# Optimization experiments

Measured on AMD Instinct MI355X. Metric: run time of the kernel, lower is better.

Reference implementation:

```python
import jax, jax.numpy as jnp
import numpy as np

N, K, D = 8192, 512, 4096

def setup_inputs() -> dict:
    key = jax.random.key(0)
    k1, k2, k3 = jax.random.split(key, 3)
    features = jax.random.normal(k1, (N, K), dtype=jnp.float32)
    w = jax.random.normal(k2, (D, N), dtype=jnp.float32)
    E = jax.random.normal(k3, (K, D), dtype=jnp.float32) / np.sqrt(K)  # embed_matrix (k x d)
    b = jnp.zeros((D,), dtype=jnp.float32)  # bias initialized to zeros in the module
    return {"features": features, "w": w, "E": E, "b": b}

def reference(features, w, E, b):
    # Linear: y = features @ E + b  -> (N, D)   (torch weight is E.mT, so x @ W.T == x @ E)
    y = features @ E + b
    # diag(y @ w): equivalent to row-wise dot products, same math without the NxN matmul
    return jnp.einsum("nd,dn->n", y, w)
```

## Files before the change

### kernel.cpp

```cpp
#include <hip/hip_runtime.h>

#define N_DIM 8192
#define K_DIM 512
#define D_DIM 4096

typedef __bf16 bf16x8 __attribute__((ext_vector_type(8)));
typedef float  f32x16 __attribute__((ext_vector_type(16)));
typedef unsigned short u16x8 __attribute__((ext_vector_type(8)));

__device__ __forceinline__ unsigned short f2bf(float f) {
    union { float f; unsigned int u; } v; v.f = f;
    unsigned int r = v.u + 0x7FFF + ((v.u >> 16) & 1);
    return (unsigned short)(r >> 16);
}

__global__ __launch_bounds__(256) void transpose_E(const float* __restrict__ E,
                                                   unsigned short* __restrict__ ETf) {
    __shared__ float tile[64][65];
    const int d0 = blockIdx.x * 64;
    const int k0 = blockIdx.y * 64;
    const int tid = threadIdx.x;
    {
        const int r  = tid / 16;
        const int c4 = (tid % 16) * 4;
#pragma unroll
        for (int p = 0; p < 4; ++p) {
            int k = p * 16 + r;
            float4 v = *reinterpret_cast<const float4*>(E + (size_t)(k0 + k) * D_DIM + d0 + c4);
            tile[k][c4 + 0] = v.x; tile[k][c4 + 1] = v.y;
            tile[k][c4 + 2] = v.z; tile[k][c4 + 3] = v.w;
        }
    }
    __syncthreads();
    const int lane = tid & 63;
    const int w    = tid >> 6;
    const int dl5  = lane & 31;
    const int k8h  = lane >> 5;
#pragma unroll
    for (int q = 0; q < 2; ++q) {
        u16x8 o;
#pragma unroll
        for (int j = 0; j < 8; ++j)
            o[j] = f2bf(tile[w * 16 + k8h * 8 + j][q * 32 + dl5]);
        const int frag = ((d0 >> 5) + q) * 32 + (k0 >> 4) + w;
        *reinterpret_cast<u16x8*>(ETf + (size_t)frag * 512 + lane * 8) = o;
    }
}

__global__ __launch_bounds__(256) void convert_F(const float* __restrict__ F,
                                                 unsigned short* __restrict__ FB) {
    const int idx8 = (blockIdx.x * 256 + threadIdx.x) * 8;
    float4 a = *reinterpret_cast<const float4*>(F + idx8);
    float4 b = *reinterpret_cast<const float4*>(F + idx8 + 4);
    u16x8 o;
    o[0] = f2bf(a.x); o[1] = f2bf(a.y); o[2] = f2bf(a.z); o[3] = f2bf(a.w);
    o[4] = f2bf(b.x); o[5] = f2bf(b.y); o[6] = f2bf(b.z); o[7] = f2bf(b.w);
    *reinterpret_cast<u16x8*>(FB + idx8) = o;
}

__global__ __launch_bounds__(256) void gemm_fused(const unsigned short* __restrict__ FB,
                                                  const float* __restrict__ W,
                                                  const unsigned short* __restrict__ ETf,
                                                  const float* __restrict__ B,
                                                  float* __restrict__ out) {
    __shared__ unsigned short Bsh[2 * 128 * 32];

    const int tid  = threadIdx.x;
    const int wave = tid >> 6;
    const int lane = tid & 63;
    const int wy   = wave >> 1;
    const int wx   = wave & 1;
    const int l31  = lane & 31;
    const int half = lane >> 5;

    const int f   = blockIdx.x + ((int)gridDim.x) * blockIdx.y;
    const int xcd = f & 7;
    const int s   = f >> 3;
    const int ntile = (xcd & 3) * 16 + (s & 15);
    const int dtile = (xcd >> 2) * 16 + (s >> 4);
    const int n0 = ntile * 128;
    const int d0 = dtile * 128;

    f32x16 acc[2][2] = {};

    const unsigned short* pa0 = ETf + (size_t)((d0 >> 5) + wy * 2 + 0) * 16384 + lane * 8;
    const unsigned short* pa1 = ETf + (size_t)((d0 >> 5) + wy * 2 + 1) * 16384 + lane * 8;

    const int srow   = lane >> 2;
    const int schunk = (((lane & 3) ^ ((srow >> 1) & 3)) * 8);

    for (int kt = 0; kt < K_DIM / 64; ++kt) {
        const int kb = kt * 64;
#pragma unroll
        for (int p = 0; p < 2; ++p) {
#pragma unroll
            for (int jj = 0; jj < 2; ++jj) {
                const int j = wave * 2 + jj;
                const unsigned short* gb =
                    FB + (size_t)(n0 + j * 16 + srow) * K_DIM + kb + p * 32 + schunk;
                __builtin_amdgcn_global_load_lds(
                    (const __attribute__((address_space(1))) void*)gb,
                    (__attribute__((address_space(3))) void*)(Bsh + p * 4096 + j * 512),
                    16, 0, 0);
            }
        }
        __syncthreads();

#pragma unroll
        for (int ks = 0; ks < 4; ++ks) {
            const int p = ks >> 1;
            const int c = (ks & 1) * 2 + half;
            bf16x8 af[2], bf[2];
            af[0] = *reinterpret_cast<const bf16x8*>(pa0 + (kt * 4 + ks) * 512);
            af[1] = *reinterpret_cast<const bf16x8*>(pa1 + (kt * 4 + ks) * 512);
#pragma unroll
            for (int ni = 0; ni < 2; ++ni) {
                const int R = wx * 64 + ni * 32 + l31;
                const int slot = c ^ ((R >> 1) & 3);
                bf[ni] = *reinterpret_cast<const bf16x8*>(
                    Bsh + p * 4096 + R * 32 + slot * 8);
            }
#pragma unroll
            for (int mi = 0; mi < 2; ++mi)
#pragma unroll
                for (int ni = 0; ni < 2; ++ni)
                    acc[mi][ni] = __builtin_amdgcn_mfma_f32_32x32x16_bf16(
                        mi == 0 ? af[0] : af[1], bf[ni], acc[mi][ni], 0, 0, 0);
        }
        __syncthreads();
    }

    const int nb = n0 + wx * 64;
    float part0 = 0.f, part1 = 0.f;
#pragma unroll
    for (int mi = 0; mi < 2; ++mi) {
        const int dbase = d0 + wy * 64 + mi * 32 + 4 * half;
#pragma unroll
        for (int reg = 0; reg < 16; ++reg) {
            const int dd = dbase + (reg & 3) + 8 * (reg >> 2);
            const float bd = B[dd];
            const float* wr = W + (size_t)dd * N_DIM + nb;
            part0 += (acc[mi][0][reg] + bd) * __builtin_nontemporal_load(wr + l31);
            part1 += (acc[mi][1][reg] + bd) * __builtin_nontemporal_load(wr + 32 + l31);
        }
    }
    part0 += __shfl_xor(part0, 32);
    part1 += __shfl_xor(part1, 32);
    if (lane < 32) {
        atomicAdd(out + nb + l31, part0);
        atomicAdd(out + nb + 32 + l31, part1);
    }
}

extern "C" void kernel_launch(void* const* d_in, const int* in_sizes, int n_in,
                              void* d_out, int out_size, void* d_ws, size_t ws_size,
                              hipStream_t stream) {
    const float* F = (const float*)d_in[0];
    const float* W = (const float*)d_in[1];
    const float* E = (const float*)d_in[2];
    const float* B = (const float*)d_in[3];
    float* out = (float*)d_out;

    unsigned short* ETf = (unsigned short*)d_ws;
    unsigned short* FB  = (unsigned short*)((char*)d_ws + (size_t)D_DIM * K_DIM * 2);

    (void)hipMemsetAsync(d_out, 0, (size_t)out_size * sizeof(float), stream);
    transpose_E<<<dim3(D_DIM / 64, K_DIM / 64), 256, 0, stream>>>(E, ETf);
    convert_F<<<dim3(N_DIM * K_DIM / (256 * 8)), 256, 0, stream>>>(F, FB);
    gemm_fused<<<dim3(N_DIM / 128, D_DIM / 128), 256, 0, stream>>>(FB, W, ETf, B, out);
}
```

Before: 244.8 us.

## Prefetch W tile into LDS during GEMM and load pre-fragmented F from global

The conversion kernel for the features now writes a bf16 copy already arranged in MFMA fragment order, so the GEMM reads B operands straight from global memory instead of staging them through LDS with barriers. The LDS freed by this holds the block's 128x128 W tile, fetched asynchronously with global_load_lds during the K loop. The epilogue then reads W from LDS, so its 64 MB stream overlaps with the matrix math instead of following it. The costs are a 64 KB LDS footprint that limits occupancy, and operand reads that no longer share data through LDS across waves.

```diff
diff --git a/kernel.cpp b/kernel.cpp
--- a/kernel.cpp
+++ b/kernel.cpp
@@ -48,22 +48,43 @@
 }
 
 __global__ __launch_bounds__(256) void convert_F(const float* __restrict__ F,
-                                                 unsigned short* __restrict__ FB) {
-    const int idx8 = (blockIdx.x * 256 + threadIdx.x) * 8;
-    float4 a = *reinterpret_cast<const float4*>(F + idx8);
-    float4 b = *reinterpret_cast<const float4*>(F + idx8 + 4);
-    u16x8 o;
-    o[0] = f2bf(a.x); o[1] = f2bf(a.y); o[2] = f2bf(a.z); o[3] = f2bf(a.w);
-    o[4] = f2bf(b.x); o[5] = f2bf(b.y); o[6] = f2bf(b.z); o[7] = f2bf(b.w);
-    *reinterpret_cast<u16x8*>(FB + idx8) = o;
+                                                 unsigned short* __restrict__ FBf) {
+    __shared__ unsigned short tl[32 * 520];
+    const int t  = threadIdx.x;
+    const int n5 = blockIdx.x;
+    const float* Fb = F + (size_t)n5 * 32 * K_DIM;
+#pragma unroll
+    for (int it = 0; it < 8; ++it) {
+        const int c  = it * 256 + t;
+        const int n  = c >> 6;
+        const int kc = (c & 63) * 8;
+        float4 a = *reinterpret_cast<const float4*>(Fb + n * K_DIM + kc);
+        float4 b = *reinterpret_cast<const float4*>(Fb + n * K_DIM + kc + 4);
+        u16x8 o;
+        o[0] = f2bf(a.x); o[1] = f2bf(a.y); o[2] = f2bf(a.z); o[3] = f2bf(a.w);
+        o[4] = f2bf(b.x); o[5] = f2bf(b.y); o[6] = f2bf(b.z); o[7] = f2bf(b.w);
+        *reinterpret_cast<u16x8*>(tl + n * 520 + kc) = o;
+    }
+    __syncthreads();
+    unsigned short* outb = FBf + (size_t)n5 * 32 * K_DIM;
+#pragma unroll
+    for (int it = 0; it < 8; ++it) {
+        const int o    = it * 256 + t;
+        const int k4   = o >> 6;
+        const int lane = o & 63;
+        const int n    = lane & 31;
+        const int kh   = (lane >> 5) * 8;
+        u16x8 v = *reinterpret_cast<const u16x8*>(tl + n * 520 + k4 * 16 + kh);
+        *reinterpret_cast<u16x8*>(outb + k4 * 512 + lane * 8) = v;
+    }
 }
 
-__global__ __launch_bounds__(256) void gemm_fused(const unsigned short* __restrict__ FB,
+__global__ __launch_bounds__(256) void gemm_fused(const unsigned short* __restrict__ FBf,
                                                   const float* __restrict__ W,
                                                   const unsigned short* __restrict__ ETf,
                                                   const float* __restrict__ B,
                                                   float* __restrict__ out) {
-    __shared__ unsigned short Bsh[2 * 128 * 32];
+    __shared__ float Wsh[128 * 128];
 
     const int tid  = threadIdx.x;
     const int wave = tid >> 6;
@@ -83,72 +104,57 @@
 
     f32x16 acc[2][2] = {};
 
-    const unsigned short* pa0 = ETf + (size_t)((d0 >> 5) + wy * 2 + 0) * 16384 + lane * 8;
-    const unsigned short* pa1 = ETf + (size_t)((d0 >> 5) + wy * 2 + 1) * 16384 + lane * 8;
+    const unsigned short* pa = ETf + (size_t)((d0 >> 5) + wy * 2) * 16384 + lane * 8;
+    const unsigned short* pb = FBf + (size_t)((n0 >> 5) + wx * 2) * 16384 + lane * 8;
 
-    const int srow   = lane >> 2;
-    const int schunk = (((lane & 3) ^ ((srow >> 1) & 3)) * 8);
+    const int wrow = lane >> 5;
+    const int wcol = (lane & 31) * 4;
 
-    for (int kt = 0; kt < K_DIM / 64; ++kt) {
-        const int kb = kt * 64;
+    for (int kt = 0; kt < 8; ++kt) {
 #pragma unroll
-        for (int p = 0; p < 2; ++p) {
-#pragma unroll
-            for (int jj = 0; jj < 2; ++jj) {
-                const int j = wave * 2 + jj;
-                const unsigned short* gb =
-                    FB + (size_t)(n0 + j * 16 + srow) * K_DIM + kb + p * 32 + schunk;
-                __builtin_amdgcn_global_load_lds(
-                    (const __attribute__((address_space(1))) void*)gb,
-                    (__attribute__((address_space(3))) void*)(Bsh + p * 4096 + j * 512),
-                    16, 0, 0);
-            }
+        for (int jj = 0; jj < 2; ++jj) {
+            const int i = kt * 8 + wave * 2 + jj;
+            const float* gw = W + (size_t)(d0 + 2 * i + wrow) * N_DIM + n0 + wcol;
+            __builtin_amdgcn_global_load_lds(
+                (const __attribute__((address_space(1))) void*)gw,
+                (__attribute__((address_space(3))) void*)(Wsh + i * 256),
+                16, 0, 2 );
         }
-        __syncthreads();
-
 #pragma unroll
         for (int ks = 0; ks < 4; ++ks) {
-            const int p = ks >> 1;
-            const int c = (ks & 1) * 2 + half;
-            bf16x8 af[2], bf[2];
-            af[0] = *reinterpret_cast<const bf16x8*>(pa0 + (kt * 4 + ks) * 512);
-            af[1] = *reinterpret_cast<const bf16x8*>(pa1 + (kt * 4 + ks) * 512);
-#pragma unroll
-            for (int ni = 0; ni < 2; ++ni) {
-                const int R = wx * 64 + ni * 32 + l31;
-                const int slot = c ^ ((R >> 1) & 3);
-                bf[ni] = *reinterpret_cast<const bf16x8*>(
-                    Bsh + p * 4096 + R * 32 + slot * 8);
-            }
-#pragma unroll
-            for (int mi = 0; mi < 2; ++mi)
-#pragma unroll
-                for (int ni = 0; ni < 2; ++ni)
-                    acc[mi][ni] = __builtin_amdgcn_mfma_f32_32x32x16_bf16(
-                        mi == 0 ? af[0] : af[1], bf[ni], acc[mi][ni], 0, 0, 0);
+            const int k16 = kt * 4 + ks;
+            bf16x8 af0 = *reinterpret_cast<const bf16x8*>(pa + (size_t)k16 * 512);
+            bf16x8 af1 = *reinterpret_cast<const bf16x8*>(pa + 16384 + (size_t)k16 * 512);
+            bf16x8 bf0 = *reinterpret_cast<const bf16x8*>(pb + (size_t)k16 * 512);
+            bf16x8 bf1 = *reinterpret_cast<const bf16x8*>(pb + 16384 + (size_t)k16 * 512);
+            acc[0][0] = __builtin_amdgcn_mfma_f32_32x32x16_bf16(af0, bf0, acc[0][0], 0, 0, 0);
+            acc[0][1] = __builtin_amdgcn_mfma_f32_32x32x16_bf16(af0, bf1, acc[0][1], 0, 0, 0);
+            acc[1][0] = __builtin_amdgcn_mfma_f32_32x32x16_bf16(af1, bf0, acc[1][0], 0, 0, 0);
+            acc[1][1] = __builtin_amdgcn_mfma_f32_32x32x16_bf16(af1, bf1, acc[1][1], 0, 0, 0);
         }
-        __syncthreads();
     }
 
-    const int nb = n0 + wx * 64;
+    __syncthreads();
+
+    const int nbl = wx * 64;
     float part0 = 0.f, part1 = 0.f;
 #pragma unroll
     for (int mi = 0; mi < 2; ++mi) {
-        const int dbase = d0 + wy * 64 + mi * 32 + 4 * half;
+        const int dlb = wy * 64 + mi * 32 + 4 * half;
 #pragma unroll
         for (int reg = 0; reg < 16; ++reg) {
-            const int dd = dbase + (reg & 3) + 8 * (reg >> 2);
-            const float bd = B[dd];
-            const float* wr = W + (size_t)dd * N_DIM + nb;
-            part0 += (acc[mi][0][reg] + bd) * __builtin_nontemporal_load(wr + l31);
-            part1 += (acc[mi][1][reg] + bd) * __builtin_nontemporal_load(wr + 32 + l31);
+            const int dl = dlb + (reg & 3) + 8 * (reg >> 2);
+            const float bd = B[d0 + dl];
+            const float* wr = Wsh + dl * 128 + nbl;
+            part0 += (acc[mi][0][reg] + bd) * wr[l31];
+            part1 += (acc[mi][1][reg] + bd) * wr[32 + l31];
         }
     }
     part0 += __shfl_xor(part0, 32);
     part1 += __shfl_xor(part1, 32);
     if (lane < 32) {
-        atomicAdd(out + nb + l31, part0);
-        atomicAdd(out + nb + 32 + l31, part1);
+        atomicAdd(out + n0 + nbl + l31, part0);
+        atomicAdd(out + n0 + nbl + 32 + l31, part1);
     }
 }
 
@@ -162,10 +168,10 @@
     float* out = (float*)d_out;
 
     unsigned short* ETf = (unsigned short*)d_ws;
-    unsigned short* FB  = (unsigned short*)((char*)d_ws + (size_t)D_DIM * K_DIM * 2);
+    unsigned short* FBf = (unsigned short*)((char*)d_ws + (size_t)D_DIM * K_DIM * 2);
 
     (void)hipMemsetAsync(d_out, 0, (size_t)out_size * sizeof(float), stream);
     transpose_E<<<dim3(D_DIM / 64, K_DIM / 64), 256, 0, stream>>>(E, ETf);
-    convert_F<<<dim3(N_DIM * K_DIM / (256 * 8)), 256, 0, stream>>>(F, FB);
-    gemm_fused<<<dim3(N_DIM / 128, D_DIM / 128), 256, 0, stream>>>(FB, W, ETf, B, out);
+    convert_F<<<dim3(N_DIM / 32), 256, 0, stream>>>(F, FBf);
+    gemm_fused<<<dim3(N_DIM / 128, D_DIM / 128), 256, 0, stream>>>(FBf, W, ETf, B, out);
 }
```

After: 245.9 us. About the same (+0.5%).
